# Kernel optimization log

Hardware: AMD Instinct MI355X
Metric: run time of the kernel (lower is better)

Reference implementation:

```python
import jax, jax.numpy as jnp
import numpy as np

B, T, IN, H, L = 32, 1024, 256, 256, 2  # batch, length, input_size, hidden_size, num_layers


def _lstm_scan(x, W_ih, W_hh, b_ih, b_hh, reverse):
    """Single-direction LSTM over time. x:[B,T,D] -> h:[B,T,H]. PyTorch gate order i,f,g,o."""
    b, t, _ = x.shape
    h_dim = W_hh.shape[1]
    # Precompute input contribution for all timesteps at once: [T,B,4H]
    xg = (jnp.einsum('btd,gd->btg', x, W_ih) + b_ih + b_hh).transpose(1, 0, 2)

    def step(carry, g_t):
        h, c = carry
        g = g_t + h @ W_hh.T
        i, f, gg, o = jnp.split(g, 4, axis=-1)
        c = jax.nn.sigmoid(f) * c + jax.nn.sigmoid(i) * jnp.tanh(gg)
        h = jax.nn.sigmoid(o) * jnp.tanh(c)
        return (h, c), h

    init = (jnp.zeros((b, h_dim), x.dtype), jnp.zeros((b, h_dim), x.dtype))
    _, hs = jax.lax.scan(step, init, xg, reverse=reverse)  # hs:[T,B,H], original time order
    return hs.transpose(1, 0, 2)


def setup_inputs() -> dict:
    key = jax.random.key(0)
    ks = iter(jax.random.split(key, 40))
    s = 1.0 / np.sqrt(H)
    inp = {'x': jax.random.normal(next(ks), (B, T, IN), jnp.float32)}
    for l in range(L):
        d_in = IN if l == 0 else 2 * H
        for dr in ('f', 'r'):
            inp[f'W_ih_{dr}{l}'] = jax.random.uniform(next(ks), (4 * H, d_in), jnp.float32, -s, s)
            inp[f'W_hh_{dr}{l}'] = jax.random.uniform(next(ks), (4 * H, H), jnp.float32, -s, s)
            inp[f'b_ih_{dr}{l}'] = jax.random.uniform(next(ks), (4 * H,), jnp.float32, -s, s)
            inp[f'b_hh_{dr}{l}'] = jax.random.uniform(next(ks), (4 * H,), jnp.float32, -s, s)
    return inp


def reference(x,
              W_ih_f0, W_hh_f0, b_ih_f0, b_hh_f0,
              W_ih_r0, W_hh_r0, b_ih_r0, b_hh_r0,
              W_ih_f1, W_hh_f1, b_ih_f1, b_hh_f1,
              W_ih_r1, W_hh_r1, b_ih_r1, b_hh_r1):
    fwd = [(W_ih_f0, W_hh_f0, b_ih_f0, b_hh_f0), (W_ih_f1, W_hh_f1, b_ih_f1, b_hh_f1)]
    rev = [(W_ih_r0, W_hh_r0, b_ih_r0, b_hh_r0), (W_ih_r1, W_hh_r1, b_ih_r1, b_hh_r1)]
    h = x
    for l in range(L):
        hf = _lstm_scan(h, *fwd[l], reverse=False)
        hr = _lstm_scan(h, *rev[l], reverse=True)
        h = jnp.concatenate([hf, hr], axis=-1)  # [B,T,2H]
    return h
```

## Files before the change

### kernel.cpp

```cpp
#include <hip/hip_runtime.h>
#include <hip/hip_fp16.h>


#define T_LEN 1024
#define BATCH 32
#define HID   256
#define G4    1024

struct __align__(16) Half8 { __half h[8]; };

typedef _Float16 f16x2 __attribute__((ext_vector_type(2)));
typedef _Float16 half8_t __attribute__((ext_vector_type(8)));
typedef float f32x4 __attribute__((ext_vector_type(4)));

__device__ __forceinline__ f16x2 pack_f16x2(float lo, float hi) {
    f16x2 r; r.x = (_Float16)lo; r.y = (_Float16)hi; return r;
}
__device__ __forceinline__ float dot2acc(f16x2 a, f16x2 b, float c) {
#if __has_builtin(__builtin_amdgcn_fdot2)
    return __builtin_amdgcn_fdot2(a, b, c, false);
#else
    return c + (float)a.x * (float)b.x + (float)a.y * (float)b.y;
#endif
}

__device__ __forceinline__ float sigm(float x) { return 1.0f / (1.0f + __expf(-x)); }
__device__ __forceinline__ float tanh_fast(float x) {
    float e = __expf(2.f * x);
    return 1.f - 2.f / (e + 1.f);
}

__global__ __launch_bounds__(256, 2) void proj_mfma(
    const float* __restrict__ A, int K,
    const float* __restrict__ Wf, const float* __restrict__ Wr,
    const float* __restrict__ bih_f, const float* __restrict__ bhh_f,
    const float* __restrict__ bih_r, const float* __restrict__ bhh_r,
    __half* __restrict__ xg)
{
    const int dir = blockIdx.z;
    const float* __restrict__ W   = dir ? Wr    : Wf;
    const float* __restrict__ bih = dir ? bih_r : bih_f;
    const float* __restrict__ bhh = dir ? bhh_r : bhh_f;
    __half* __restrict__ outp = xg + (size_t)dir * ((size_t)BATCH * T_LEN * G4);

    __shared__ char psm[36864];
    __half* As = (__half*)psm;
    __half* Bs = (__half*)(psm + 18432);

    const int tid  = threadIdx.x;
    const int lane = tid & 63;
    const int wave = tid >> 6;
    const int wm   = wave >> 1;
    const int wn   = wave & 1;
    const int fr   = lane & 15;
    const int fk   = lane >> 4;
    const int m0   = blockIdx.y * 128;
    const int n0   = blockIdx.x * 128;

    float biasv[4];
    #pragma unroll
    for (int ni = 0; ni < 4; ++ni) {
        int n = n0 + wn * 64 + ni * 16 + fr;
        biasv[ni] = bih[n] + bhh[n];
    }

    f32x4 acc[4][4];
    #pragma unroll
    for (int mi = 0; mi < 4; ++mi)
        #pragma unroll
        for (int ni = 0; ni < 4; ++ni)
            acc[mi][ni] = (f32x4){0.f, 0.f, 0.f, 0.f};

    for (int k0 = 0; k0 < K; k0 += 64) {
        #pragma unroll
        for (int it = 0; it < 4; ++it) {
            int t2  = tid + it * 256;
            int row = t2 >> 3;
            int ks  = (t2 & 7) * 8;
            const float* pa = &A[(size_t)(m0 + row) * K + k0 + ks];
            const float* pb = &W[(size_t)(n0 + row) * K + k0 + ks];
            float4 a0 = *reinterpret_cast<const float4*>(pa);
            float4 a1 = *reinterpret_cast<const float4*>(pa + 4);
            float4 b0 = *reinterpret_cast<const float4*>(pb);
            float4 b1 = *reinterpret_cast<const float4*>(pb + 4);
            Half8 ha, hb;
            ha.h[0] = __float2half(a0.x); ha.h[1] = __float2half(a0.y);
            ha.h[2] = __float2half(a0.z); ha.h[3] = __float2half(a0.w);
            ha.h[4] = __float2half(a1.x); ha.h[5] = __float2half(a1.y);
            ha.h[6] = __float2half(a1.z); ha.h[7] = __float2half(a1.w);
            hb.h[0] = __float2half(b0.x); hb.h[1] = __float2half(b0.y);
            hb.h[2] = __float2half(b0.z); hb.h[3] = __float2half(b0.w);
            hb.h[4] = __float2half(b1.x); hb.h[5] = __float2half(b1.y);
            hb.h[6] = __float2half(b1.z); hb.h[7] = __float2half(b1.w);
            *reinterpret_cast<Half8*>(&As[row * 72 + ks]) = ha;
            *reinterpret_cast<Half8*>(&Bs[row * 72 + ks]) = hb;
        }
        __syncthreads();

        #pragma unroll
        for (int kk = 0; kk < 2; ++kk) {
            half8_t af[4], bf[4];
            #pragma unroll
            for (int mi = 0; mi < 4; ++mi)
                af[mi] = *reinterpret_cast<const half8_t*>(
                    &As[(wm * 64 + mi * 16 + fr) * 72 + kk * 32 + fk * 8]);
            #pragma unroll
            for (int ni = 0; ni < 4; ++ni)
                bf[ni] = *reinterpret_cast<const half8_t*>(
                    &Bs[(wn * 64 + ni * 16 + fr) * 72 + kk * 32 + fk * 8]);
            #pragma unroll
            for (int mi = 0; mi < 4; ++mi)
                #pragma unroll
                for (int ni = 0; ni < 4; ++ni)
                    acc[mi][ni] = __builtin_amdgcn_mfma_f32_16x16x32_f16(
                        af[mi], bf[ni], acc[mi][ni], 0, 0, 0);
        }
        __syncthreads();
    }

    __half* Cs = (__half*)psm;
    #pragma unroll
    for (int mi = 0; mi < 4; ++mi)
        #pragma unroll
        for (int ni = 0; ni < 4; ++ni) {
            #pragma unroll
            for (int i = 0; i < 4; ++i) {
                int row = wm * 64 + mi * 16 + fk * 4 + i;
                int col = wn * 64 + ni * 16 + fr;
                Cs[row * 136 + col] = __float2half(acc[mi][ni][i] + biasv[ni]);
            }
        }
    __syncthreads();
    #pragma unroll
    for (int it = 0; it < 8; ++it) {
        int slot = it * 256 + tid;
        int row  = slot >> 4;
        int c8   = (slot & 15) * 8;
        Half8 v = *reinterpret_cast<const Half8*>(&Cs[row * 136 + c8]);
        *reinterpret_cast<Half8*>(&outp[(size_t)(m0 + row) * G4 + n0 + c8]) = v;
    }
}

extern "C" __global__ __launch_bounds__(512, 2) void recur10_kernel(
    const __half* __restrict__ xg,
    const float* __restrict__ Whh_f,
    const float* __restrict__ Whh_r,
    float* __restrict__ outp,
    unsigned long long* __restrict__ hbt,
    unsigned int tagbase)
{
    __shared__ char smem[55296];
    __half* hl  = (__half*)smem;
    float*  scr = (float*)(smem + 1024);

    const int tid = threadIdx.x;
    const int bid = blockIdx.x;
    const int jq  = bid >> 6;
    const int d   = (bid >> 5) & 1;
    const int b   = bid & 31;
    const float* __restrict__ Whh = d ? Whh_r : Whh_f;

    const int kh = tid >> 8;
    const int r  = tid & 255;
    const int q  = r >> 6;
    const int jl = r & 63;
    const int n_my = (q << 8) + jq * 64 + jl;

    unsigned wh[64];
    {
        const float* wrow = Whh + (size_t)n_my * HID + kh * 128;
        #pragma unroll
        for (int i = 0; i < 32; ++i) {
            float4 w4 = *reinterpret_cast<const float4*>(&wrow[i * 4]);
            wh[2 * i]     = __builtin_bit_cast(unsigned, pack_f16x2(w4.x, w4.y));
            wh[2 * i + 1] = __builtin_bit_cast(unsigned, pack_f16x2(w4.z, w4.w));
        }
    }
    #pragma unroll
    for (int i = 0; i < 64; ++i) asm volatile("" : "+v"(wh[i]));

    unsigned long long* hb = hbt + (size_t)(d * 32 + b) * 512;

    if (tid < 64) {
        __hip_atomic_store(&hb[256 + jq * 64 + tid],
                           (unsigned long long)tagbase << 32,
                           __ATOMIC_RELAXED, __HIP_MEMORY_SCOPE_AGENT);
        hl[0 * 256 + jq * 64 + tid] = __float2half(0.f);
    }

    const bool isPoll = (tid >= 256) && (tid < 448);
    int pslot = 0;
    if (isPoll) {
        int u  = tid - 256;
        int fq = u >> 6;
        int qq = fq + (fq >= jq);
        pslot  = qq * 64 + (u & 63);
    }

    const __half* __restrict__ xgp =
        xg + ((size_t)(d * BATCH + b)) * T_LEN * G4 + n_my;

    float c_state = 0.f;

    for (int st = 0; st < T_LEN; ++st) {
        const int t = d ? (T_LEN - 1 - st) : st;

        float xv = (kh == 0) ? __half2float(xgp[(size_t)t * G4]) : 0.f;

        __half* hlcur = hl + (st & 1) * 256;

        if (isPoll) {
            const unsigned int exp = tagbase + (unsigned)st;
            unsigned long long* src = hb + (size_t)((st + 1) & 1) * 256 + pslot;
            unsigned long long v =
                __hip_atomic_load(src, __ATOMIC_RELAXED, __HIP_MEMORY_SCOPE_AGENT);
            while ((unsigned int)(v >> 32) != exp)
                v = __hip_atomic_load(src, __ATOMIC_RELAXED, __HIP_MEMORY_SCOPE_AGENT);
            hlcur[pslot] = __float2half(__uint_as_float((unsigned int)v));
        }
        __syncthreads();

        float a0 = xv, a1 = 0.f;
        {
            const float4* hp = reinterpret_cast<const float4*>(hlcur + kh * 128);
            #pragma unroll
            for (int i = 0; i < 16; ++i) {
                float4 hv = hp[i];
                a0 = dot2acc(__builtin_bit_cast(f16x2, hv.x), __builtin_bit_cast(f16x2, wh[4 * i + 0]), a0);
                a1 = dot2acc(__builtin_bit_cast(f16x2, hv.y), __builtin_bit_cast(f16x2, wh[4 * i + 1]), a1);
                a0 = dot2acc(__builtin_bit_cast(f16x2, hv.z), __builtin_bit_cast(f16x2, wh[4 * i + 2]), a0);
                a1 = dot2acc(__builtin_bit_cast(f16x2, hv.w), __builtin_bit_cast(f16x2, wh[4 * i + 3]), a1);
            }
        }
        scr[kh * 256 + r] = a0 + a1;
        __syncthreads();

        if (tid < 64) {
            float gi = scr[      tid] + scr[256 +       tid];
            float gf = scr[ 64 + tid] + scr[256 +  64 + tid];
            float gg = scr[128 + tid] + scr[256 + 128 + tid];
            float go = scr[192 + tid] + scr[256 + 192 + tid];
            float ii = sigm(gi);
            float ff = sigm(gf);
            float g2 = tanh_fast(gg);
            float oo = sigm(go);
            c_state = ff * c_state + ii * g2;
            float h = oo * tanh_fast(c_state);
            const int j = jq * 64 + tid;
            hl[((st + 1) & 1) * 256 + j] = __float2half(h);
            unsigned long long pv =
                ((unsigned long long)(tagbase + (unsigned)st + 1u) << 32) | __float_as_uint(h);
            __hip_atomic_store(&hb[(size_t)(st & 1) * 256 + j], pv,
                               __ATOMIC_RELAXED, __HIP_MEMORY_SCOPE_AGENT);
            outp[((size_t)b * T_LEN + t) * (2 * HID) + d * HID + j] = h;
        }
    }
}

extern "C" void kernel_launch(void* const* d_in, const int* in_sizes, int n_in,
                              void* d_out, int out_size, void* d_ws, size_t ws_size,
                              hipStream_t stream)
{
    const float* x       = (const float*)d_in[0];
    const float* W_ih_f0 = (const float*)d_in[1];
    const float* W_hh_f0 = (const float*)d_in[2];
    const float* b_ih_f0 = (const float*)d_in[3];
    const float* b_hh_f0 = (const float*)d_in[4];
    const float* W_ih_r0 = (const float*)d_in[5];
    const float* W_hh_r0 = (const float*)d_in[6];
    const float* b_ih_r0 = (const float*)d_in[7];
    const float* b_hh_r0 = (const float*)d_in[8];
    const float* W_ih_f1 = (const float*)d_in[9];
    const float* W_hh_f1 = (const float*)d_in[10];
    const float* b_ih_f1 = (const float*)d_in[11];
    const float* b_hh_f1 = (const float*)d_in[12];
    const float* W_ih_r1 = (const float*)d_in[13];
    const float* W_hh_r1 = (const float*)d_in[14];
    const float* b_ih_r1 = (const float*)d_in[15];
    const float* b_hh_r1 = (const float*)d_in[16];

    float* outp = (float*)d_out;

    __half* xg = (__half*)d_ws;
    const size_t xg_bytes = (size_t)2 * BATCH * T_LEN * G4 * sizeof(__half);
    unsigned long long* hbt = (unsigned long long*)((char*)d_ws + xg_bytes);

    hipMemsetAsync(hbt, 0, 262144, stream);

    proj_mfma<<<dim3(8, 256, 2), 256, 0, stream>>>(x, 256, W_ih_f0, W_ih_r0,
        b_ih_f0, b_hh_f0, b_ih_r0, b_hh_r0, xg);
    {
        const __half* xg_c = xg;
        unsigned int base0 = 1u;
        void* args[] = {(void*)&xg_c, (void*)&W_hh_f0, (void*)&W_hh_r0,
                        (void*)&outp, (void*)&hbt, (void*)&base0};
        hipLaunchCooperativeKernel(reinterpret_cast<const void*>(recur10_kernel),
                                   dim3(256), dim3(512), args, 0, stream);
    }

    proj_mfma<<<dim3(8, 256, 2), 256, 0, stream>>>(outp, 512, W_ih_f1, W_ih_r1,
        b_ih_f1, b_hh_f1, b_ih_r1, b_hh_r1, xg);
    {
        const __half* xg_c = xg;
        unsigned int base1 = 4096u;
        void* args[] = {(void*)&xg_c, (void*)&W_hh_f1, (void*)&W_hh_r1,
                        (void*)&outp, (void*)&hbt, (void*)&base1};
        hipLaunchCooperativeKernel(reinterpret_cast<const void*>(recur10_kernel),
                                   dim3(256), dim3(512), args, 0, stream);
    }
}
```

Before: 2.992 ms.

## Pack two batch rows per block and overlap their LSTM recurrence steps

```diff
diff --git a/kernel.cpp b/kernel.cpp
--- a/kernel.cpp
+++ b/kernel.cpp
@@ -24,11 +24,20 @@
 #endif
 }
 
+template <int CTRL>
+__device__ __forceinline__ float qpermf(float v) {
+    int i = __builtin_bit_cast(int, v);
+    int r = __builtin_amdgcn_update_dpp(i, i, CTRL, 0xF, 0xF, true);
+    return __builtin_bit_cast(float, r);
+}
+
 __device__ __forceinline__ float sigm(float x) { return 1.0f / (1.0f + __expf(-x)); }
 __device__ __forceinline__ float tanh_fast(float x) {
     float e = __expf(2.f * x);
     return 1.f - 2.f / (e + 1.f);
 }
+
+#define WQ(q, i) __builtin_bit_cast(f16x2, wq[q][i])
 
 __global__ __launch_bounds__(256, 2) void proj_mfma(
     const float* __restrict__ A, int K,
@@ -141,7 +150,7 @@
     }
 }
 
-extern "C" __global__ __launch_bounds__(512, 2) void recur10_kernel(
+extern "C" __global__ __launch_bounds__(512, 2) void recur13_kernel(
     const __half* __restrict__ xg,
     const float* __restrict__ Whh_f,
     const float* __restrict__ Whh_r,
@@ -149,113 +158,181 @@
     unsigned long long* __restrict__ hbt,
     unsigned int tagbase)
 {
-    __shared__ char smem[55296];
-    __half* hl  = (__half*)smem;
-    float*  scr = (float*)(smem + 1024);
+    extern __shared__ char smem[];
+    __half* hl = (__half*)smem;
 
     const int tid = threadIdx.x;
     const int bid = blockIdx.x;
-    const int jq  = bid >> 6;
-    const int d   = (bid >> 5) & 1;
-    const int b   = bid & 31;
+    const int jq  = bid >> 5;
+    const int d   = (bid >> 4) & 1;
+    const int bp  = bid & 15;
     const float* __restrict__ Whh = d ? Whh_r : Whh_f;
 
-    const int kh = tid >> 8;
-    const int r  = tid & 255;
-    const int q  = r >> 6;
-    const int jl = r & 63;
-    const int n_my = (q << 8) + jq * 64 + jl;
-
-    unsigned wh[64];
-    {
-        const float* wrow = Whh + (size_t)n_my * HID + kh * 128;
-        #pragma unroll
-        for (int i = 0; i < 32; ++i) {
+    const int lb = tid >> 8;
+    const int u  = tid & 255;
+    const int j  = u >> 2;
+    const int ks = u & 3;
+    const int b  = bp * 2 + lb;
+    const int cell_my = jq * 64 + j;
+
+    unsigned wq[4][32];
+    #pragma unroll
+    for (int q = 0; q < 4; ++q) {
+        const float* wrow = Whh + (size_t)((q << 8) + cell_my) * HID + ks * 64;
+        #pragma unroll
+        for (int i = 0; i < 16; ++i) {
             float4 w4 = *reinterpret_cast<const float4*>(&wrow[i * 4]);
-            wh[2 * i]     = __builtin_bit_cast(unsigned, pack_f16x2(w4.x, w4.y));
-            wh[2 * i + 1] = __builtin_bit_cast(unsigned, pack_f16x2(w4.z, w4.w));
-        }
-    }
-    #pragma unroll
-    for (int i = 0; i < 64; ++i) asm volatile("" : "+v"(wh[i]));
-
-    unsigned long long* hb = hbt + (size_t)(d * 32 + b) * 512;
-
-    if (tid < 64) {
-        __hip_atomic_store(&hb[256 + jq * 64 + tid],
-                           (unsigned long long)tagbase << 32,
+            wq[q][2 * i]     = __builtin_bit_cast(unsigned, pack_f16x2(w4.x, w4.y));
+            wq[q][2 * i + 1] = __builtin_bit_cast(unsigned, pack_f16x2(w4.z, w4.w));
+        }
+    }
+    #pragma unroll
+    for (int q = 0; q < 4; ++q)
+        #pragma unroll
+        for (int i = 0; i < 32; ++i)
+            asm volatile("" : "+v"(wq[q][i]));
+
+    unsigned long long* hb0 = hbt + (size_t)(d * 32 + bp * 2) * 512;
+    unsigned long long* hb1 = hb0 + 512;
+
+    if (tid < 128) {
+        int lbi = tid >> 6;
+        int c = jq * 64 + (tid & 63);
+        unsigned long long* hbx = lbi ? hb1 : hb0;
+        __hip_atomic_store(&hbx[256 + c], (unsigned long long)tagbase << 32,
                            __ATOMIC_RELAXED, __HIP_MEMORY_SCOPE_AGENT);
-        hl[0 * 256 + jq * 64 + tid] = __float2half(0.f);
-    }
-
-    const bool isPoll = (tid >= 256) && (tid < 448);
-    int pslot = 0;
-    if (isPoll) {
-        int u  = tid - 256;
-        int fq = u >> 6;
-        int qq = fq + (fq >= jq);
-        pslot  = qq * 64 + (u & 63);
-    }
+        hl[((lbi * 2 + 0) * 4 + jq) * 72 + (tid & 63)] = __float2half(0.f);
+    }
+    if (tid < 192) {
+        int fq = tid >> 6, qq = fq + (fq >= jq), c = qq * 64 + (tid & 63);
+        unsigned long long* src = &hb0[256 + c];
+        unsigned long long v = __hip_atomic_load(src, __ATOMIC_RELAXED, __HIP_MEMORY_SCOPE_AGENT);
+        while ((unsigned)(v >> 32) != tagbase)
+            v = __hip_atomic_load(src, __ATOMIC_RELAXED, __HIP_MEMORY_SCOPE_AGENT);
+        hl[((0 * 2 + 0) * 4 + (c >> 6)) * 72 + (c & 63)] =
+            __float2half(__uint_as_float((unsigned)v));
+    }
+    __syncthreads();
 
     const __half* __restrict__ xgp =
-        xg + ((size_t)(d * BATCH + b)) * T_LEN * G4 + n_my;
+        xg + ((size_t)(d * BATCH + b)) * T_LEN * G4 + ((ks << 8) + cell_my);
 
     float c_state = 0.f;
 
     for (int st = 0; st < T_LEN; ++st) {
         const int t = d ? (T_LEN - 1 - st) : st;
-
-        float xv = (kh == 0) ? __half2float(xgp[(size_t)t * G4]) : 0.f;
-
-        __half* hlcur = hl + (st & 1) * 256;
-
-        if (isPoll) {
-            const unsigned int exp = tagbase + (unsigned)st;
-            unsigned long long* src = hb + (size_t)((st + 1) & 1) * 256 + pslot;
-            unsigned long long v =
-                __hip_atomic_load(src, __ATOMIC_RELAXED, __HIP_MEMORY_SCOPE_AGENT);
-            while ((unsigned int)(v >> 32) != exp)
+        const int par = st & 1;
+
+        float xv = __half2float(xgp[(size_t)t * G4]);
+
+        if (tid < 256) {
+            float a0 = 0.f, a1 = 0.f, a2 = 0.f, a3 = 0.f;
+            const float4* hp = reinterpret_cast<const float4*>(
+                hl + (size_t)((0 * 2 + par) * 4 + ks) * 72);
+            #pragma unroll
+            for (int i = 0; i < 8; ++i) {
+                float4 hv = hp[i];
+                f16x2 h0 = __builtin_bit_cast(f16x2, hv.x);
+                f16x2 h1 = __builtin_bit_cast(f16x2, hv.y);
+                f16x2 h2 = __builtin_bit_cast(f16x2, hv.z);
+                f16x2 h3 = __builtin_bit_cast(f16x2, hv.w);
+                a0 = dot2acc(h0, WQ(0, 4*i+0), a0); a0 = dot2acc(h1, WQ(0, 4*i+1), a0);
+                a0 = dot2acc(h2, WQ(0, 4*i+2), a0); a0 = dot2acc(h3, WQ(0, 4*i+3), a0);
+                a1 = dot2acc(h0, WQ(1, 4*i+0), a1); a1 = dot2acc(h1, WQ(1, 4*i+1), a1);
+                a1 = dot2acc(h2, WQ(1, 4*i+2), a1); a1 = dot2acc(h3, WQ(1, 4*i+3), a1);
+                a2 = dot2acc(h0, WQ(2, 4*i+0), a2); a2 = dot2acc(h1, WQ(2, 4*i+1), a2);
+                a2 = dot2acc(h2, WQ(2, 4*i+2), a2); a2 = dot2acc(h3, WQ(2, 4*i+3), a2);
+                a3 = dot2acc(h0, WQ(3, 4*i+0), a3); a3 = dot2acc(h1, WQ(3, 4*i+1), a3);
+                a3 = dot2acc(h2, WQ(3, 4*i+2), a3); a3 = dot2acc(h3, WQ(3, 4*i+3), a3);
+            }
+            if      (ks == 0) a0 += xv;
+            else if (ks == 1) a1 += xv;
+            else if (ks == 2) a2 += xv;
+            else              a3 += xv;
+            a0 += qpermf<0xB1>(a0); a0 += qpermf<0x4E>(a0);
+            a1 += qpermf<0xB1>(a1); a1 += qpermf<0x4E>(a1);
+            a2 += qpermf<0xB1>(a2); a2 += qpermf<0x4E>(a2);
+            a3 += qpermf<0xB1>(a3); a3 += qpermf<0x4E>(a3);
+            if (ks == 0) {
+                float ii = sigm(a0), ff = sigm(a1);
+                float g2 = tanh_fast(a2), oo = sigm(a3);
+                c_state = ff * c_state + ii * g2;
+                float h = oo * tanh_fast(c_state);
+                unsigned long long pv =
+                    ((unsigned long long)(tagbase + (unsigned)st + 1u) << 32) | __float_as_uint(h);
+                __hip_atomic_store(&hb0[(size_t)par * 256 + cell_my], pv,
+                                   __ATOMIC_RELAXED, __HIP_MEMORY_SCOPE_AGENT);
+                hl[((0 * 2 + (par ^ 1)) * 4 + jq) * 72 + j] = __float2half(h);
+                outp[((size_t)b * T_LEN + t) * (2 * HID) + d * HID + cell_my] = h;
+            }
+        } else if (tid < 448) {
+            int u2 = tid - 256;
+            int fq = u2 >> 6, qq = fq + (fq >= jq), c = qq * 64 + (u2 & 63);
+            unsigned long long* src = &hb1[(size_t)(par ^ 1) * 256 + c];
+            const unsigned exp = tagbase + (unsigned)st;
+            unsigned long long v = __hip_atomic_load(src, __ATOMIC_RELAXED, __HIP_MEMORY_SCOPE_AGENT);
+            while ((unsigned)(v >> 32) != exp)
                 v = __hip_atomic_load(src, __ATOMIC_RELAXED, __HIP_MEMORY_SCOPE_AGENT);
-            hlcur[pslot] = __float2half(__uint_as_float((unsigned int)v));
+            hl[((1 * 2 + par) * 4 + (c >> 6)) * 72 + (c & 63)] =
+                __float2half(__uint_as_float((unsigned)v));
         }
         __syncthreads();
 
-        float a0 = xv, a1 = 0.f;
-        {
-            const float4* hp = reinterpret_cast<const float4*>(hlcur + kh * 128);
-            #pragma unroll
-            for (int i = 0; i < 16; ++i) {
+        if (tid >= 256) {
+            float a0 = 0.f, a1 = 0.f, a2 = 0.f, a3 = 0.f;
+            const float4* hp = reinterpret_cast<const float4*>(
+                hl + (size_t)((1 * 2 + par) * 4 + ks) * 72);
+            #pragma unroll
+            for (int i = 0; i < 8; ++i) {
                 float4 hv = hp[i];
-                a0 = dot2acc(__builtin_bit_cast(f16x2, hv.x), __builtin_bit_cast(f16x2, wh[4 * i + 0]), a0);
-                a1 = dot2acc(__builtin_bit_cast(f16x2, hv.y), __builtin_bit_cast(f16x2, wh[4 * i + 1]), a1);
-                a0 = dot2acc(__builtin_bit_cast(f16x2, hv.z), __builtin_bit_cast(f16x2, wh[4 * i + 2]), a0);
-                a1 = dot2acc(__builtin_bit_cast(f16x2, hv.w), __builtin_bit_cast(f16x2, wh[4 * i + 3]), a1);
-            }
-        }
-        scr[kh * 256 + r] = a0 + a1;
+                f16x2 h0 = __builtin_bit_cast(f16x2, hv.x);
+                f16x2 h1 = __builtin_bit_cast(f16x2, hv.y);
+                f16x2 h2 = __builtin_bit_cast(f16x2, hv.z);
+                f16x2 h3 = __builtin_bit_cast(f16x2, hv.w);
+                a0 = dot2acc(h0, WQ(0, 4*i+0), a0); a0 = dot2acc(h1, WQ(0, 4*i+1), a0);
+                a0 = dot2acc(h2, WQ(0, 4*i+2), a0); a0 = dot2acc(h3, WQ(0, 4*i+3), a0);
+                a1 = dot2acc(h0, WQ(1, 4*i+0), a1); a1 = dot2acc(h1, WQ(1, 4*i+1), a1);
+                a1 = dot2acc(h2, WQ(1, 4*i+2), a1); a1 = dot2acc(h3, WQ(1, 4*i+3), a1);
+                a2 = dot2acc(h0, WQ(2, 4*i+0), a2); a2 = dot2acc(h1, WQ(2, 4*i+1), a2);
+                a2 = dot2acc(h2, WQ(2, 4*i+2), a2); a2 = dot2acc(h3, WQ(2, 4*i+3), a2);
+                a3 = dot2acc(h0, WQ(3, 4*i+0), a3); a3 = dot2acc(h1, WQ(3, 4*i+1), a3);
+                a3 = dot2acc(h2, WQ(3, 4*i+2), a3); a3 = dot2acc(h3, WQ(3, 4*i+3), a3);
+            }
+            if      (ks == 0) a0 += xv;
+            else if (ks == 1) a1 += xv;
+            else if (ks == 2) a2 += xv;
+            else              a3 += xv;
+            a0 += qpermf<0xB1>(a0); a0 += qpermf<0x4E>(a0);
+            a1 += qpermf<0xB1>(a1); a1 += qpermf<0x4E>(a1);
+            a2 += qpermf<0xB1>(a2); a2 += qpermf<0x4E>(a2);
+            a3 += qpermf<0xB1>(a3); a3 += qpermf<0x4E>(a3);
+            if (ks == 0) {
+                float ii = sigm(a0), ff = sigm(a1);
+                float g2 = tanh_fast(a2), oo = sigm(a3);
+                c_state = ff * c_state + ii * g2;
+                float h = oo * tanh_fast(c_state);
+                unsigned long long pv =
+                    ((unsigned long long)(tagbase + (unsigned)st + 1u) << 32) | __float_as_uint(h);
+                __hip_atomic_store(&hb1[(size_t)par * 256 + cell_my], pv,
+                                   __ATOMIC_RELAXED, __HIP_MEMORY_SCOPE_AGENT);
+                hl[((1 * 2 + (par ^ 1)) * 4 + jq) * 72 + j] = __float2half(h);
+                outp[((size_t)b * T_LEN + t) * (2 * HID) + d * HID + cell_my] = h;
+            }
+        } else if (tid < 192 && st < T_LEN - 1) {
+            int fq = tid >> 6, qq = fq + (fq >= jq), c = qq * 64 + (tid & 63);
+            unsigned long long* src = &hb0[(size_t)par * 256 + c];
+            const unsigned exp = tagbase + (unsigned)st + 1u;
+            unsigned long long v = __hip_atomic_load(src, __ATOMIC_RELAXED, __HIP_MEMORY_SCOPE_AGENT);
+            while ((unsigned)(v >> 32) != exp)
+                v = __hip_atomic_load(src, __ATOMIC_RELAXED, __HIP_MEMORY_SCOPE_AGENT);
+            hl[((0 * 2 + (par ^ 1)) * 4 + (c >> 6)) * 72 + (c & 63)] =
+                __float2half(__uint_as_float((unsigned)v));
+        }
         __syncthreads();
-
-        if (tid < 64) {
-            float gi = scr[      tid] + scr[256 +       tid];
-            float gf = scr[ 64 + tid] + scr[256 +  64 + tid];
-            float gg = scr[128 + tid] + scr[256 + 128 + tid];
-            float go = scr[192 + tid] + scr[256 + 192 + tid];
-            float ii = sigm(gi);
-            float ff = sigm(gf);
-            float g2 = tanh_fast(gg);
-            float oo = sigm(go);
-            c_state = ff * c_state + ii * g2;
-            float h = oo * tanh_fast(c_state);
-            const int j = jq * 64 + tid;
-            hl[((st + 1) & 1) * 256 + j] = __float2half(h);
-            unsigned long long pv =
-                ((unsigned long long)(tagbase + (unsigned)st + 1u) << 32) | __float_as_uint(h);
-            __hip_atomic_store(&hb[(size_t)(st & 1) * 256 + j], pv,
-                               __ATOMIC_RELAXED, __HIP_MEMORY_SCOPE_AGENT);
-            outp[((size_t)b * T_LEN + t) * (2 * HID) + d * HID + j] = h;
-        }
-    }
-}
+    }
+}
+
+#define RECUR_LDS 98304u
 
 extern "C" void kernel_launch(void* const* d_in, const int* in_sizes, int n_in,
                               void* d_out, int out_size, void* d_ws, size_t ws_size,
@@ -285,6 +362,9 @@
     const size_t xg_bytes = (size_t)2 * BATCH * T_LEN * G4 * sizeof(__half);
     unsigned long long* hbt = (unsigned long long*)((char*)d_ws + xg_bytes);
 
+    hipFuncSetAttribute(reinterpret_cast<const void*>(recur13_kernel),
+                        hipFuncAttributeMaxDynamicSharedMemorySize, RECUR_LDS);
+
     hipMemsetAsync(hbt, 0, 262144, stream);
 
     proj_mfma<<<dim3(8, 256, 2), 256, 0, stream>>>(x, 256, W_ih_f0, W_ih_r0,
@@ -294,8 +374,8 @@
         unsigned int base0 = 1u;
         void* args[] = {(void*)&xg_c, (void*)&W_hh_f0, (void*)&W_hh_r0,
                         (void*)&outp, (void*)&hbt, (void*)&base0};
-        hipLaunchCooperativeKernel(reinterpret_cast<const void*>(recur10_kernel),
-                                   dim3(256), dim3(512), args, 0, stream);
+        hipLaunchCooperativeKernel(reinterpret_cast<const void*>(recur13_kernel),
+                                   dim3(128), dim3(512), args, RECUR_LDS, stream);
     }
 
     proj_mfma<<<dim3(8, 256, 2), 256, 0, stream>>>(outp, 512, W_ih_f1, W_ih_r1,
@@ -305,7 +385,7 @@
         unsigned int base1 = 4096u;
         void* args[] = {(void*)&xg_c, (void*)&W_hh_f1, (void*)&W_hh_r1,
                         (void*)&outp, (void*)&hbt, (void*)&base1};
-        hipLaunchCooperativeKernel(reinterpret_cast<const void*>(recur10_kernel),
-                                   dim3(256), dim3(512), args, 0, stream);
-    }
-}
+        hipLaunchCooperativeKernel(reinterpret_cast<const void*>(recur13_kernel),
+                                   dim3(128), dim3(512), args, RECUR_LDS, stream);
+    }
+}
```

Result: slower. 3.658 ms (+22.2%).
